# Kernel tuning notes

Hardware: AMD Instinct MI355X
Metric: run time of the kernel (lower is better)

The kernel has to match this reference:

```python
import jax, jax.numpy as jnp
import numpy as np

B = 4; RESO = 64; VIT = 16; PAD = 0.1; TRI_C = 64; IMG_C = 1280
INNER = 128; OUT_C = 64; HEADS = 8; NIMG = 5
N_TRI = 3 * RESO * RESO  # 12288 triplane locations


def pos_enc(d_model, length):
    pos = jnp.arange(length, dtype=jnp.float32)[:, None]
    div = jnp.exp(jnp.arange(0, d_model, 2, dtype=jnp.float32) * (-np.log(10000.0) / d_model))
    pe = jnp.zeros((length, d_model), jnp.float32)
    pe = pe.at[:, 0::2].set(jnp.sin(pos * div)).at[:, 1::2].set(jnp.cos(pos * div))
    return pe


def triplane_coords():
    ar = jnp.arange(RESO, dtype=jnp.float32)
    A, Bm = jnp.meshgrid(ar, ar, indexing='xy')  # matches torch indexing='xy'
    half = jnp.full_like(A, (RESO - 1) / 2.0)
    xz = jnp.stack([A, half, Bm], -1)
    xy = jnp.stack([A, Bm, half], -1)
    yz = jnp.stack([half, A, Bm], -1)
    c = jnp.concatenate([xz, xy, yz], 0).reshape(-1, 3)
    c = c / (RESO - 1)
    return (c - 0.5) * 2.0 * (1.0 + PAD + 1e-05)  # [N_TRI, 3]


def trilinear_sample(vol, grid):
    # vol [B,C,D,H,W]; grid [B,M,3] in [-1,1] as (x->W, y->H, z->D); align_corners=True
    Bv, C, D, H, W = vol.shape
    gx, gy, gz = grid[..., 0], grid[..., 1], grid[..., 2]
    ix = (gx + 1.0) * 0.5 * (W - 1)
    iy = (gy + 1.0) * 0.5 * (H - 1)
    iz = (gz + 1.0) * 0.5 * (D - 1)
    x0 = jnp.floor(ix); y0 = jnp.floor(iy); z0 = jnp.floor(iz)
    wx = ix - x0; wy = iy - y0; wz = iz - z0
    x0i = jnp.clip(x0.astype(jnp.int32), 0, W - 1); x1i = jnp.clip(x0i + 1, 0, W - 1)
    y0i = jnp.clip(y0.astype(jnp.int32), 0, H - 1); y1i = jnp.clip(y0i + 1, 0, H - 1)
    z0i = jnp.clip(z0.astype(jnp.int32), 0, D - 1); z1i = jnp.clip(z0i + 1, 0, D - 1)
    vf = vol.reshape(Bv, C, D * H * W)
    def g(zi, yi, xi):
        idx = (zi * H + yi) * W + xi  # [B,M]
        return jnp.take_along_axis(vf, idx[:, None, :], axis=2)  # [B,C,M]
    out = 0.0
    for zi, wz_ in ((z0i, 1.0 - wz), (z1i, wz)):
        for yi, wy_ in ((y0i, 1.0 - wy), (y1i, wy)):
            for xi, wx_ in ((x0i, 1.0 - wx), (x1i, wx)):
                out = out + g(zi, yi, xi) * (wz_ * wy_ * wx_)[:, None, :]
    return out  # [B,C,M]


def _forward(triplane_feat, image_feat, proj_mat, k_w, k_b, q_w, q_b, v_w, v_b,
             in_w, in_b, out_w, out_b, conv_w, conv_b, valid_frames):
    Bb, n_img = image_feat.shape[0], image_feat.shape[1]
    img = image_feat[:, :, 1:, :]  # drop CLS -> [B,n,256,1280]
    pe_img = pos_enc(INNER, VIT * VIT)  # [256,128]
    kimg = img @ k_w.T + k_b + pe_img
    vimg = img @ v_w.T + v_b + pe_img
    kv = jnp.concatenate([kimg, vimg], -1)  # [B,n,256,2E]
    vol = kv.reshape(Bb, n_img, VIT, VIT, 2 * INNER).transpose(0, 4, 1, 2, 3)  # [B,2E,D,H,W]

    coords = triplane_coords()
    homo = jnp.concatenate([coords, jnp.ones((N_TRI, 1), jnp.float32)], -1)  # [N,4]
    cin = jnp.einsum('nc,bjkc->bjnk', homo, proj_mat)  # == homo @ proj^T
    x = cin[..., 0] / cin[..., 2] / (224.0 - 1)
    y = cin[..., 1] / cin[..., 2] / (224.0 - 1)
    xy = (jnp.stack([x, y], -1) - 0.5) * 2.0
    gi = (jnp.arange(n_img, dtype=jnp.float32) / (n_img - 1) - 0.5) * 2.0
    gi = jnp.broadcast_to(gi[None, :, None, None], (Bb, n_img, N_TRI, 1))
    grid = jnp.clip(jnp.concatenate([xy, gi], -1), -1.0, 1.0)  # [B,n,N,3]

    samp = trilinear_sample(vol, grid.reshape(Bb, n_img * N_TRI, 3))
    samp = samp.reshape(Bb, 2 * INNER, n_img, N_TRI)
    kk = samp[:, :INNER].transpose(0, 3, 2, 1)  # [B,N,n,E]
    vv = samp[:, INNER:].transpose(0, 3, 2, 1)

    tq = triplane_feat.reshape(Bb, TRI_C, N_TRI).transpose(0, 2, 1)  # b (h w) c
    q = tq @ q_w.T + q_b + pos_enc(INNER, N_TRI)

    E, dh = INNER, INNER // HEADS
    Wq, Wk, Wv = in_w[:E], in_w[E:2 * E], in_w[2 * E:]
    bq, bk, bv = in_b[:E], in_b[E:2 * E], in_b[2 * E:]
    qp = (q @ Wq.T + bq).reshape(Bb, N_TRI, HEADS, dh)
    kp = (kk @ Wk.T + bk).reshape(Bb, N_TRI, n_img, HEADS, dh)
    vp = (vv @ Wv.T + bv).reshape(Bb, N_TRI, n_img, HEADS, dh)
    scores = jnp.einsum('bnhd,bnjhd->bnhj', qp, kp) / np.sqrt(dh).astype(np.float32)
    attn = jax.nn.softmax(scores, axis=-1)
    o = jnp.einsum('bnhj,bnjhd->bnhd', attn, vp).reshape(Bb, N_TRI, E)
    o = o @ out_w.T + out_b  # [B,N,E]

    t = o.transpose(0, 2, 1).reshape(Bb, E, 3 * RESO, RESO)
    return jnp.einsum('bchw,oc->bohw', t, conv_w) + conv_b[None, :, None, None]


def setup_inputs() -> dict:
    key = jax.random.key(0)
    ks = jax.random.split(key, 16)
    s = 0.02
    pm = jax.random.normal(ks[2], (B, NIMG, 4, 4), jnp.float32)
    proj = pm * 30.0  # pixel-scale projection rows
    zrow = jnp.concatenate([pm[..., 2, :3] * 0.05, 3.0 + 0.5 * jnp.abs(pm[..., 2, 3:4])], -1)
    proj_mat = proj.at[..., 2, :].set(zrow)  # positive depth, safe division
    return {
        'triplane_feat': jax.random.normal(ks[0], (B, TRI_C, 3 * RESO, RESO), jnp.float32),
        'image_feat': jax.random.normal(ks[1], (B, NIMG, VIT * VIT + 1, IMG_C), jnp.float32),
        'proj_mat': proj_mat,
        'valid_frames': jnp.ones((B, NIMG), jnp.int32),
        'k_w': jax.random.normal(ks[3], (INNER, IMG_C), jnp.float32) * s,
        'k_b': jnp.zeros((INNER,), jnp.float32),
        'q_w': jax.random.normal(ks[4], (INNER, TRI_C), jnp.float32) * s,
        'q_b': jnp.zeros((INNER,), jnp.float32),
        'v_w': jax.random.normal(ks[5], (INNER, IMG_C), jnp.float32) * s,
        'v_b': jnp.zeros((INNER,), jnp.float32),
        'in_w': jax.random.normal(ks[6], (3 * INNER, INNER), jnp.float32) * s,
        'in_b': jnp.zeros((3 * INNER,), jnp.float32),
        'out_w': jax.random.normal(ks[7], (INNER, INNER), jnp.float32) * s,
        'out_b': jnp.zeros((INNER,), jnp.float32),
        'conv_w': jax.random.normal(ks[8], (OUT_C, INNER), jnp.float32) * s,
        'conv_b': jnp.zeros((OUT_C,), jnp.float32),
    }


def reference(triplane_feat, image_feat, proj_mat, valid_frames, k_w, k_b, q_w, q_b,
              v_w, v_b, in_w, in_b, out_w, out_b, conv_w, conv_b):
    return _forward(triplane_feat, image_feat, proj_mat, k_w, k_b, q_w, q_b, v_w, v_b,
                    in_w, in_b, out_w, out_b, conv_w, conv_b, valid_frames)
```

## Files before the change

### kernel.cpp

```cpp
#include <hip/hip_runtime.h>
#include <math.h>

#define NTRI 12288

#define OFF_WT    0u
#define OFF_PEKV  327680u
#define OFF_CQWT  393216u
#define OFF_PEQ   401408u
#define OFF_W2T   1974272u
#define OFF_B2    1982464u
#define OFF_INWT  1982528u
#define OFF_KVPV  2031680u
#define OFF_GTAB  3342400u

typedef short short8 __attribute__((ext_vector_type(8)));
typedef float f32x4 __attribute__((ext_vector_type(4)));

__device__ __forceinline__ unsigned short f2bf(float f) {
  unsigned u = __float_as_uint(f);
  return (unsigned short)((u + 0x7fff + ((u >> 16) & 1)) >> 16);
}
__device__ __forceinline__ float bflo(unsigned u) {
  return __uint_as_float(u << 16);
}
__device__ __forceinline__ float bfhi(unsigned u) {
  return __uint_as_float(u & 0xffff0000u);
}

__global__ __launch_bounds__(256) void k_inwT(const float* __restrict__ in_w,
                                              float* __restrict__ inwT) {
  int idx = blockIdx.x * 256 + threadIdx.x;
  int r = idx >> 7, m = idx & 127;
  inwT[m * 384 + r] = in_w[idx];
}

__global__ __launch_bounds__(256) void k_pre(const float* __restrict__ inwT,
    const float* __restrict__ k_w, const float* __restrict__ v_w,
    const float* __restrict__ k_b, const float* __restrict__ v_b,
    const float* __restrict__ in_b, const float* __restrict__ q_w,
    const float* __restrict__ q_b, const float* __restrict__ conv_w,
    const float* __restrict__ out_w, const float* __restrict__ out_b,
    const float* __restrict__ conv_b, const float* __restrict__ proj,
    unsigned short* __restrict__ wTc, float* __restrict__ pekv,
    float* __restrict__ cqwT, float* __restrict__ peq,
    float* __restrict__ w2t, float* __restrict__ b2,
    float4* __restrict__ gtab) {
  __shared__ float spe8[8][128];
  __shared__ float skv[256];
  int bb = blockIdx.x;
  int t = threadIdx.x;

  if (bb < 1280) {
    int i = bb, c = t;
    if (t < 128) skv[t] = k_w[(size_t)t * 1280 + i];
    else         skv[t] = v_w[(size_t)(t - 128) * 1280 + i];
    __syncthreads();
    const float* sp = (c < 128) ? skv : (skv + 128);
    float acc = 0.f;
    for (int m = 0; m < 128; ++m)
      acc += inwT[m * 384 + 128 + c] * sp[m];
    wTc[(size_t)c * 1280 + i] = f2bf(acc);
  } else if (bb < 1536) {
    int p = bb - 1280;
    if (t < 128) {
      float dv = __expf(-(float)(t & ~1) * (9.210340371976184f / 128.0f));
      float arg = (float)p * dv;
      spe8[0][t] = (t & 1) ? cosf(arg) : sinf(arg);
    }
    __syncthreads();
    const float* bias = (t < 128) ? k_b : v_b;
    float acc = 0.f;
    for (int m = 0; m < 128; ++m)
      acc += inwT[m * 384 + 128 + t] * (bias[m] + spe8[0][m]);
    pekv[p * 256 + t] = acc + in_b[128 + t];
  } else if (bb < 1568) {
    int idx = (bb - 1536) * 256 + t;
    int k = idx >> 7, c = idx & 127;
    float acc = 0.f;
    for (int m = 0; m < 128; ++m)
      acc += inwT[m * 384 + c] * q_w[m * 64 + k];
    cqwT[idx] = acc;
  } else if (bb < 3104) {
    int n8 = (bb - 1568) * 8;
    for (int it = 0; it < 4; ++it) {
      int e = it * 256 + t;
      int nn = e >> 7, m = e & 127;
      float dv = __expf(-(float)(m & ~1) * (9.210340371976184f / 128.0f));
      float arg = (float)(n8 + nn) * dv;
      spe8[nn][m] = q_b[m] + ((m & 1) ? cosf(arg) : sinf(arg));
    }
    __syncthreads();
    int c = t & 127, z = t >> 7;
    float a0 = 0, a1 = 0, a2 = 0, a3 = 0;
    for (int m = 0; m < 128; ++m) {
      float w = inwT[m * 384 + c];
      a0 += w * spe8[z * 4 + 0][m];
      a1 += w * spe8[z * 4 + 1][m];
      a2 += w * spe8[z * 4 + 2][m];
      a3 += w * spe8[z * 4 + 3][m];
    }
    float bbv = in_b[c];
    peq[(n8 + z * 4 + 0) * 128 + c] = a0 + bbv;
    peq[(n8 + z * 4 + 1) * 128 + c] = a1 + bbv;
    peq[(n8 + z * 4 + 2) * 128 + c] = a2 + bbv;
    peq[(n8 + z * 4 + 3) * 128 + c] = a3 + bbv;
  } else if (bb < 3137) {
    int idx = (bb - 3104) * 256 + t;
    if (idx < 8192) {
      int c = idx >> 6, oc = idx & 63;
      float acc = 0.f;
      for (int m = 0; m < 128; ++m)
        acc += conv_w[oc * 128 + m] * out_w[m * 128 + c];
      w2t[c * 64 + oc] = acc;
    } else if (idx < 8256) {
      int oc = idx - 8192;
      float acc = 0.f;
      for (int m = 0; m < 128; ++m)
        acc += conv_w[oc * 128 + m] * out_b[m];
      b2[oc] = acc + conv_b[oc];
    }
  } else {
    int idx = (bb - 3137) * 256 + t;
    int n = idx % NTRI;
    int bj = idx / NTRI;
    int plane = n >> 12, rem = n & 4095;
    float fa = (float)(rem & 63), fb = (float)(rem >> 6);
    float cx, cy, cz;
    if (plane == 0)      { cx = fa;    cy = 31.5f; cz = fb; }
    else if (plane == 1) { cx = fa;    cy = fb;    cz = 31.5f; }
    else                 { cx = 31.5f; cy = fa;    cz = fb; }
    const float s2 = 2.20002f;
    cx = (cx / 63.0f - 0.5f) * s2;
    cy = (cy / 63.0f - 0.5f) * s2;
    cz = (cz / 63.0f - 0.5f) * s2;
    const float* P = &proj[bj * 16];
    float d0 = cx * P[0] + cy * P[1] + cz * P[2] + P[3];
    float d1 = cx * P[4] + cy * P[5] + cz * P[6] + P[7];
    float d2 = cx * P[8] + cy * P[9] + cz * P[10] + P[11];
    float x = d0 / d2 / 223.0f;
    float y = d1 / d2 / 223.0f;
    float gx = fminf(fmaxf((x - 0.5f) * 2.0f, -1.0f), 1.0f);
    float gy = fminf(fmaxf((y - 0.5f) * 2.0f, -1.0f), 1.0f);
    float ix = (gx + 1.0f) * 7.5f, iy = (gy + 1.0f) * 7.5f;
    float fx = floorf(ix), fy = floorf(iy);
    float wx = ix - fx, wy = iy - fy;
    int x0 = (int)fx; x0 = x0 < 0 ? 0 : (x0 > 15 ? 15 : x0);
    int y0 = (int)fy; y0 = y0 < 0 ? 0 : (y0 > 15 ? 15 : y0);
    int x1 = x0 + 1 > 15 ? 15 : x0 + 1;
    int y1 = y0 + 1 > 15 ? 15 : y0 + 1;
    int pack = x0 | (x1 << 8) | (y0 << 16) | (y1 << 24);
    gtab[idx] = make_float4(wx, wy, __int_as_float(pack), 0.f);
  }
}

#define LDA 72
__global__ __launch_bounds__(256) void k_kv(const float* __restrict__ img,
    const unsigned short* __restrict__ wTc, const float* __restrict__ pekv,
    unsigned short* __restrict__ kv16) {
  __shared__ unsigned short sA[32 * LDA];
  __shared__ unsigned short sB[64 * LDA];
  int t = threadIdx.x;
  int gm = blockIdx.x >> 2;
  int gn = blockIdx.x & 3;
  int r0 = gm * 32, c0 = gn * 64;
  int lane = t & 63, w = t >> 6;
  int wm = w & 1, wn = w >> 1;
  int lrow = lane & 15, quad = lane >> 4;
  int srow = t >> 3, schunk = t & 7;
  int bj = gm >> 3;
  f32x4 acc0 = {0,0,0,0}, acc1 = {0,0,0,0};

  float4 pA0, pA1;
  short8 pB0, pB1;
  auto issue = [&](int kt) {
    int k0 = kt * 64;
    const float4* s = (const float4*)&img[(size_t)(r0 + srow + bj + 1) * 1280 + k0 + schunk * 8];
    pA0 = s[0]; pA1 = s[1];
    pB0 = *(const short8*)&wTc[(size_t)(c0 + srow) * 1280 + k0 + schunk * 8];
    pB1 = *(const short8*)&wTc[(size_t)(c0 + srow + 32) * 1280 + k0 + schunk * 8];
  };
  issue(0);

  for (int kt = 0; kt < 20; ++kt) {
    __syncthreads();
    {
      short8 av;
      av[0] = (short)f2bf(pA0.x); av[1] = (short)f2bf(pA0.y);
      av[2] = (short)f2bf(pA0.z); av[3] = (short)f2bf(pA0.w);
      av[4] = (short)f2bf(pA1.x); av[5] = (short)f2bf(pA1.y);
      av[6] = (short)f2bf(pA1.z); av[7] = (short)f2bf(pA1.w);
      *(short8*)&sA[srow * LDA + schunk * 8] = av;
      *(short8*)&sB[srow * LDA + schunk * 8] = pB0;
      *(short8*)&sB[(srow + 32) * LDA + schunk * 8] = pB1;
    }
    __syncthreads();
    if (kt < 19) issue(kt + 1);
#pragma unroll
    for (int kk = 0; kk < 2; ++kk) {
      int kof = kk * 32 + quad * 8;
      short8 a  = *(const short8*)&sA[(wm * 16 + lrow) * LDA + kof];
      short8 b0 = *(const short8*)&sB[(wn * 32 + lrow) * LDA + kof];
      short8 b1 = *(const short8*)&sB[(wn * 32 + 16 + lrow) * LDA + kof];
      acc0 = __builtin_amdgcn_mfma_f32_16x16x32_bf16(a, b0, acc0, 0, 0, 0);
      acc1 = __builtin_amdgcn_mfma_f32_16x16x32_bf16(a, b1, acc1, 0, 0, 0);
    }
  }
  f32x4 accs[2] = {acc0, acc1};
#pragma unroll
  for (int ni = 0; ni < 2; ++ni)
#pragma unroll
    for (int r = 0; r < 4; ++r) {
      int grow = r0 + wm * 16 + quad * 4 + r;
      int gcol = c0 + wn * 32 + ni * 16 + lrow;
      kv16[(size_t)grow * 256 + gcol] =
          f2bf(accs[ni][r] + pekv[(grow & 255) * 256 + gcol]);
    }
}

__global__ __launch_bounds__(256, 2) void k_main(const float* __restrict__ tri,
    const float* __restrict__ cqwT, const float* __restrict__ peq,
    const float* __restrict__ w2t, const float* __restrict__ b2,
    const unsigned short* __restrict__ kv16, const float4* __restrict__ gtab,
    float* __restrict__ outp) {
  __shared__ float smem[32 * 132 + 64 * 36];
  float* sQP = smem;
  float* sO2 = smem;
  float* sTQ = smem + 32 * 132;
  float* sFO = smem + 32 * 132;

  int t = threadIdx.x;
  int lane = t & 63, w = t >> 6;
  int b = blockIdx.x / 384;
  int n0 = (blockIdx.x % 384) * 32;

  for (int it = 0; it < 8; ++it) {
    int e = it * 256 + t;
    int k = e >> 5, pt = e & 31;
    sTQ[k * 36 + pt] = tri[(size_t)(b * 64 + k) * NTRI + n0 + pt];
  }
  __syncthreads();

  {
    int c4 = (t & 31) * 4;
    int p4 = (t >> 5) * 4;
    const float* cw = cqwT + c4;
    float4 A0 = {0,0,0,0}, A1 = {0,0,0,0}, A2 = {0,0,0,0}, A3 = {0,0,0,0};
#pragma unroll 4
    for (int k = 0; k < 64; ++k) {
      float4 wv = *(const float4*)(cw + k * 128);
      float4 aq = *(const float4*)&sTQ[k * 36 + p4];
      A0.x += aq.x * wv.x; A0.y += aq.x * wv.y; A0.z += aq.x * wv.z; A0.w += aq.x * wv.w;
      A1.x += aq.y * wv.x; A1.y += aq.y * wv.y; A1.z += aq.y * wv.z; A1.w += aq.y * wv.w;
      A2.x += aq.z * wv.x; A2.y += aq.z * wv.y; A2.z += aq.z * wv.z; A2.w += aq.z * wv.w;
      A3.x += aq.w * wv.x; A3.y += aq.w * wv.y; A3.z += aq.w * wv.z; A3.w += aq.w * wv.w;
    }
    float4 acc[4] = {A0, A1, A2, A3};
#pragma unroll
    for (int pp = 0; pp < 4; ++pp) {
      float4 pe = *(const float4*)&peq[(size_t)(n0 + p4 + pp) * 128 + c4];
      float4 r;
      r.x = acc[pp].x + pe.x; r.y = acc[pp].y + pe.y;
      r.z = acc[pp].z + pe.z; r.w = acc[pp].w + pe.w;
      *(float4*)&sQP[(p4 + pp) * 132 + c4] = r;
    }
  }
  __syncthreads();

  {
    int sub = lane & 31, half = lane >> 5, c4 = sub * 4;
    const unsigned short* Vb = kv16 + (size_t)b * 5 * 65536;
    const float4* gbase = &gtab[(size_t)(b * 5) * NTRI];
    for (int s = 0; s < 4; ++s) {
      int pt = s * 8 + w * 2 + half;
      int n = n0 + pt;
      float4 qp4 = *(const float4*)&sQP[pt * 132 + c4];
      float4 gp[5];
#pragma unroll
      for (int j = 0; j < 5; ++j) gp[j] = gbase[(size_t)j * NTRI + n];
      float4 vst[5];
      float sc[5];
#pragma unroll
      for (int j = 0; j < 5; ++j) {
        int pack = __float_as_int(gp[j].z);
        int x0 = pack & 255, x1 = (pack >> 8) & 255;
        int y0 = (pack >> 16) & 255, y1 = (pack >> 24) & 255;
        float wx = gp[j].x, wy = gp[j].y;
        const unsigned short* r0 = Vb + j * 65536 + y0 * 4096;
        const unsigned short* r1 = Vb + j * 65536 + y1 * 4096;
        int i0 = x0 * 256 + c4, i1 = x1 * 256 + c4;
        uint2 K00 = *(const uint2*)(r0 + i0), K01 = *(const uint2*)(r0 + i1);
        uint2 K10 = *(const uint2*)(r1 + i0), K11 = *(const uint2*)(r1 + i1);
        uint2 V00 = *(const uint2*)(r0 + i0 + 128), V01 = *(const uint2*)(r0 + i1 + 128);
        uint2 V10 = *(const uint2*)(r1 + i0 + 128), V11 = *(const uint2*)(r1 + i1 + 128);
        float w00 = (1.f - wx) * (1.f - wy), w01 = wx * (1.f - wy);
        float w10 = (1.f - wx) * wy, w11 = wx * wy;
        float4 kc, vc;
        kc.x = bflo(K00.x) * w00 + bflo(K01.x) * w01 + bflo(K10.x) * w10 + bflo(K11.x) * w11;
        kc.y = bfhi(K00.x) * w00 + bfhi(K01.x) * w01 + bfhi(K10.x) * w10 + bfhi(K11.x) * w11;
        kc.z = bflo(K00.y) * w00 + bflo(K01.y) * w01 + bflo(K10.y) * w10 + bflo(K11.y) * w11;
        kc.w = bfhi(K00.y) * w00 + bfhi(K01.y) * w01 + bfhi(K10.y) * w10 + bfhi(K11.y) * w11;
        vc.x = bflo(V00.x) * w00 + bflo(V01.x) * w01 + bflo(V10.x) * w10 + bflo(V11.x) * w11;
        vc.y = bfhi(V00.x) * w00 + bfhi(V01.x) * w01 + bfhi(V10.x) * w10 + bfhi(V11.x) * w11;
        vc.z = bflo(V00.y) * w00 + bflo(V01.y) * w01 + bflo(V10.y) * w10 + bflo(V11.y) * w11;
        vc.w = bfhi(V00.y) * w00 + bfhi(V01.y) * w01 + bfhi(V10.y) * w10 + bfhi(V11.y) * w11;
        vst[j] = vc;
        float pa = qp4.x * kc.x + qp4.y * kc.y + qp4.z * kc.z + qp4.w * kc.w;
        pa += __shfl_xor(pa, 1);
        pa += __shfl_xor(pa, 2);
        sc[j] = pa * 0.25f;
      }
      float mx = fmaxf(fmaxf(fmaxf(sc[0], sc[1]), fmaxf(sc[2], sc[3])), sc[4]);
      float e0 = expf(sc[0] - mx), e1 = expf(sc[1] - mx), e2 = expf(sc[2] - mx);
      float e3 = expf(sc[3] - mx), e4 = expf(sc[4] - mx);
      float inv = 1.0f / (e0 + e1 + e2 + e3 + e4);
      float4 oa;
      oa.x = (e0 * vst[0].x + e1 * vst[1].x + e2 * vst[2].x + e3 * vst[3].x + e4 * vst[4].x) * inv;
      oa.y = (e0 * vst[0].y + e1 * vst[1].y + e2 * vst[2].y + e3 * vst[3].y + e4 * vst[4].y) * inv;
      oa.z = (e0 * vst[0].z + e1 * vst[1].z + e2 * vst[2].z + e3 * vst[3].z + e4 * vst[4].z) * inv;
      oa.w = (e0 * vst[0].w + e1 * vst[1].w + e2 * vst[2].w + e3 * vst[3].w + e4 * vst[4].w) * inv;
      *(float4*)&sO2[pt * 132 + c4] = oa;
    }
  }
  __syncthreads();

  {
    int oc4 = (t & 15) * 4;
    int pg = t >> 4;
    float f00 = 0, f01 = 0, f02 = 0, f03 = 0;
    float f10 = 0, f11 = 0, f12 = 0, f13 = 0;
    const float* o0 = &sO2[(pg * 2) * 132];
    const float* o1 = &sO2[(pg * 2 + 1) * 132];
#pragma unroll 8
    for (int cc = 0; cc < 128; ++cc) {
      float4 wv = *(const float4*)&w2t[cc * 64 + oc4];
      float ax = o0[cc], ay = o1[cc];
      f00 += ax * wv.x; f01 += ax * wv.y; f02 += ax * wv.z; f03 += ax * wv.w;
      f10 += ay * wv.x; f11 += ay * wv.y; f12 += ay * wv.z; f13 += ay * wv.w;
    }
    float4 bb = *(const float4*)&b2[oc4];
    int p0 = pg * 2, p1 = pg * 2 + 1;
    sFO[(oc4 + 0) * 33 + p0] = f00 + bb.x; sFO[(oc4 + 0) * 33 + p1] = f10 + bb.x;
    sFO[(oc4 + 1) * 33 + p0] = f01 + bb.y; sFO[(oc4 + 1) * 33 + p1] = f11 + bb.y;
    sFO[(oc4 + 2) * 33 + p0] = f02 + bb.z; sFO[(oc4 + 2) * 33 + p1] = f12 + bb.z;
    sFO[(oc4 + 3) * 33 + p0] = f03 + bb.w; sFO[(oc4 + 3) * 33 + p1] = f13 + bb.w;
  }
  __syncthreads();

  for (int it = 0; it < 8; ++it) {
    int e = it * 256 + t;
    int oc = e >> 5, pt = e & 31;
    outp[(size_t)(b * 64 + oc) * NTRI + n0 + pt] = sFO[oc * 33 + pt];
  }
}

extern "C" void kernel_launch(void* const* d_in, const int* in_sizes, int n_in,
                              void* d_out, int out_size, void* d_ws, size_t ws_size,
                              hipStream_t stream) {
  const float* tri    = (const float*)d_in[0];
  const float* img    = (const float*)d_in[1];
  const float* proj   = (const float*)d_in[2];
  const float* k_w    = (const float*)d_in[4];
  const float* k_b    = (const float*)d_in[5];
  const float* q_w    = (const float*)d_in[6];
  const float* q_b    = (const float*)d_in[7];
  const float* v_w    = (const float*)d_in[8];
  const float* v_b    = (const float*)d_in[9];
  const float* in_w   = (const float*)d_in[10];
  const float* in_b   = (const float*)d_in[11];
  const float* out_w  = (const float*)d_in[12];
  const float* out_b  = (const float*)d_in[13];
  const float* conv_w = (const float*)d_in[14];
  const float* conv_b = (const float*)d_in[15];
  float* ws = (float*)d_ws;
  unsigned short* wTc  = (unsigned short*)(ws + OFF_WT);
  float* pekv = ws + OFF_PEKV;
  float* cqwT = ws + OFF_CQWT;
  float* peq  = ws + OFF_PEQ;
  float* w2t  = ws + OFF_W2T;
  float* b2   = ws + OFF_B2;
  float* inwT = ws + OFF_INWT;
  unsigned short* kv16 = (unsigned short*)(ws + OFF_KVPV);
  float* gtab = ws + OFF_GTAB;
  float* outp = (float*)d_out;

  k_inwT<<<192, 256, 0, stream>>>(in_w, inwT);
  k_pre<<<4097, 256, 0, stream>>>(inwT, k_w, v_w, k_b, v_b, in_b, q_w, q_b,
                                  conv_w, out_w, out_b, conv_b, proj,
                                  wTc, pekv, cqwT, peq, w2t, b2, (float4*)gtab);
  k_kv<<<640, 256, 0, stream>>>(img, wTc, pekv, kv16);
  k_main<<<1536, 256, 0, stream>>>(tri, cqwT, peq, w2t, b2, kv16,
                                   (const float4*)gtab, outp);
}
```

Measured before the change: 218.5 us.

## Interleave K/V bf16 layout and use online softmax in bilinear attention gather

The KV projection kernel now writes K and V channels interleaved in groups of four, so each lane fetches its K and V slices with one 16-byte load per corner instead of two 8-byte loads. The main kernel computes the Q·K dot per corner before bilinear weighting, and replaces the stored-then-normalized softmax over 5 views with an online running-max softmax in a non-unrolled loop. The aim is fewer, wider gather loads and lower register pressure. The cost is extra exp calls and serialized loads across views, which reduces memory-level parallelism.

```diff
diff --git a/kernel.cpp b/kernel.cpp
--- a/kernel.cpp
+++ b/kernel.cpp
@@ -212,7 +212,9 @@
     for (int r = 0; r < 4; ++r) {
       int grow = r0 + wm * 16 + quad * 4 + r;
       int gcol = c0 + wn * 32 + ni * 16 + lrow;
-      kv16[(size_t)grow * 256 + gcol] =
+      int ncol = (gcol < 128) ? (((gcol >> 2) << 3) | (gcol & 3))
+                              : ((((gcol - 128) >> 2) << 3) | 4 | (gcol & 3));
+      kv16[(size_t)grow * 256 + ncol] =
           f2bf(accs[ni][r] + pekv[(grow & 255) * 256 + gcol]);
     }
 }
@@ -274,50 +276,50 @@
       int pt = s * 8 + w * 2 + half;
       int n = n0 + pt;
       float4 qp4 = *(const float4*)&sQP[pt * 132 + c4];
-      float4 gp[5];
-#pragma unroll
-      for (int j = 0; j < 5; ++j) gp[j] = gbase[(size_t)j * NTRI + n];
-      float4 vst[5];
-      float sc[5];
-#pragma unroll
+      float m = -1e30f, den = 0.f;
+      float oax = 0.f, oay = 0.f, oaz = 0.f, oaw = 0.f;
+#pragma unroll 1
       for (int j = 0; j < 5; ++j) {
-        int pack = __float_as_int(gp[j].z);
+        float4 g = gbase[(size_t)j * NTRI + n];
+        int pack = __float_as_int(g.z);
         int x0 = pack & 255, x1 = (pack >> 8) & 255;
         int y0 = (pack >> 16) & 255, y1 = (pack >> 24) & 255;
-        float wx = gp[j].x, wy = gp[j].y;
+        float wx = g.x, wy = g.y;
         const unsigned short* r0 = Vb + j * 65536 + y0 * 4096;
         const unsigned short* r1 = Vb + j * 65536 + y1 * 4096;
-        int i0 = x0 * 256 + c4, i1 = x1 * 256 + c4;
-        uint2 K00 = *(const uint2*)(r0 + i0), K01 = *(const uint2*)(r0 + i1);
-        uint2 K10 = *(const uint2*)(r1 + i0), K11 = *(const uint2*)(r1 + i1);
-        uint2 V00 = *(const uint2*)(r0 + i0 + 128), V01 = *(const uint2*)(r0 + i1 + 128);
-        uint2 V10 = *(const uint2*)(r1 + i0 + 128), V11 = *(const uint2*)(r1 + i1 + 128);
+        int i0 = x0 * 256 + sub * 8, i1 = x1 * 256 + sub * 8;
+        uint4 Q00 = *(const uint4*)(r0 + i0), Q01 = *(const uint4*)(r0 + i1);
+        uint4 Q10 = *(const uint4*)(r1 + i0), Q11 = *(const uint4*)(r1 + i1);
         float w00 = (1.f - wx) * (1.f - wy), w01 = wx * (1.f - wy);
         float w10 = (1.f - wx) * wy, w11 = wx * wy;
-        float4 kc, vc;
-        kc.x = bflo(K00.x) * w00 + bflo(K01.x) * w01 + bflo(K10.x) * w10 + bflo(K11.x) * w11;
-        kc.y = bfhi(K00.x) * w00 + bfhi(K01.x) * w01 + bfhi(K10.x) * w10 + bfhi(K11.x) * w11;
-        kc.z = bflo(K00.y) * w00 + bflo(K01.y) * w01 + bflo(K10.y) * w10 + bflo(K11.y) * w11;
-        kc.w = bfhi(K00.y) * w00 + bfhi(K01.y) * w01 + bfhi(K10.y) * w10 + bfhi(K11.y) * w11;
-        vc.x = bflo(V00.x) * w00 + bflo(V01.x) * w01 + bflo(V10.x) * w10 + bflo(V11.x) * w11;
-        vc.y = bfhi(V00.x) * w00 + bfhi(V01.x) * w01 + bfhi(V10.x) * w10 + bfhi(V11.x) * w11;
-        vc.z = bflo(V00.y) * w00 + bflo(V01.y) * w01 + bflo(V10.y) * w10 + bflo(V11.y) * w11;
-        vc.w = bfhi(V00.y) * w00 + bfhi(V01.y) * w01 + bfhi(V10.y) * w10 + bfhi(V11.y) * w11;
-        vst[j] = vc;
-        float pa = qp4.x * kc.x + qp4.y * kc.y + qp4.z * kc.z + qp4.w * kc.w;
+        float d00 = bflo(Q00.x) * qp4.x + bfhi(Q00.x) * qp4.y
+                  + bflo(Q00.y) * qp4.z + bfhi(Q00.y) * qp4.w;
+        float d01 = bflo(Q01.x) * qp4.x + bfhi(Q01.x) * qp4.y
+                  + bflo(Q01.y) * qp4.z + bfhi(Q01.y) * qp4.w;
+        float d10 = bflo(Q10.x) * qp4.x + bfhi(Q10.x) * qp4.y
+                  + bflo(Q10.y) * qp4.z + bfhi(Q10.y) * qp4.w;
+        float d11 = bflo(Q11.x) * qp4.x + bfhi(Q11.x) * qp4.y
+                  + bflo(Q11.y) * qp4.z + bfhi(Q11.y) * qp4.w;
+        float pa = d00 * w00 + d01 * w01 + d10 * w10 + d11 * w11;
         pa += __shfl_xor(pa, 1);
         pa += __shfl_xor(pa, 2);
-        sc[j] = pa * 0.25f;
+        float sj = pa * 0.25f;
+        float vcx = bflo(Q00.z) * w00 + bflo(Q01.z) * w01 + bflo(Q10.z) * w10 + bflo(Q11.z) * w11;
+        float vcy = bfhi(Q00.z) * w00 + bfhi(Q01.z) * w01 + bfhi(Q10.z) * w10 + bfhi(Q11.z) * w11;
+        float vcz = bflo(Q00.w) * w00 + bflo(Q01.w) * w01 + bflo(Q10.w) * w10 + bflo(Q11.w) * w11;
+        float vcw = bfhi(Q00.w) * w00 + bfhi(Q01.w) * w01 + bfhi(Q10.w) * w10 + bfhi(Q11.w) * w11;
+        float mn = fmaxf(m, sj);
+        float rr = expf(m - mn);
+        float ee = expf(sj - mn);
+        den = den * rr + ee;
+        oax = oax * rr + ee * vcx;
+        oay = oay * rr + ee * vcy;
+        oaz = oaz * rr + ee * vcz;
+        oaw = oaw * rr + ee * vcw;
+        m = mn;
       }
-      float mx = fmaxf(fmaxf(fmaxf(sc[0], sc[1]), fmaxf(sc[2], sc[3])), sc[4]);
-      float e0 = expf(sc[0] - mx), e1 = expf(sc[1] - mx), e2 = expf(sc[2] - mx);
-      float e3 = expf(sc[3] - mx), e4 = expf(sc[4] - mx);
-      float inv = 1.0f / (e0 + e1 + e2 + e3 + e4);
-      float4 oa;
-      oa.x = (e0 * vst[0].x + e1 * vst[1].x + e2 * vst[2].x + e3 * vst[3].x + e4 * vst[4].x) * inv;
-      oa.y = (e0 * vst[0].y + e1 * vst[1].y + e2 * vst[2].y + e3 * vst[3].y + e4 * vst[4].y) * inv;
-      oa.z = (e0 * vst[0].z + e1 * vst[1].z + e2 * vst[2].z + e3 * vst[3].z + e4 * vst[4].z) * inv;
-      oa.w = (e0 * vst[0].w + e1 * vst[1].w + e2 * vst[2].w + e3 * vst[3].w + e4 * vst[4].w) * inv;
+      float inv = 1.0f / den;
+      float4 oa = make_float4(oax * inv, oay * inv, oaz * inv, oaw * inv);
       *(float4*)&sO2[pt * 132 + c4] = oa;
     }
   }
```

Result: faster. 214.0 us (-2.1%).
